# Kernel tuning notes

Hardware: AMD Instinct MI355X
Metric: run time of the kernel (lower is better)

The kernel has to match this reference:

```python
import jax, jax.numpy as jnp
import numpy as np

N_SVC, N_NODE, N_POD = 50000, 20000, 100000
F = 128          # svc/instance/node feature dims (all 128 per init_kwargs)
HID = 128        # hidden_size
OUT = 64         # out_channel
E_SVC, E_PN, E_NP = 1600000, 100000, 100000


def _graph_conv(x, src, dst, n_src, n_dst, W, b):
    """DGL GraphConv with norm='both': D_dst^{-1/2} A D_src^{-1/2} X W + b."""
    ones = jnp.ones(src.shape[0], dtype=x.dtype)
    deg_src = jnp.clip(jax.ops.segment_sum(ones, src, num_segments=n_src), 1.0)
    deg_dst = jnp.clip(jax.ops.segment_sum(ones, dst, num_segments=n_dst), 1.0)
    # normalize at source, gather, scatter-sum to dst, normalize at dst
    h = x * jax.lax.rsqrt(deg_src)[:, None]          # [n_src, F]
    msg = h[src]                                      # [E, F] gather (memory-bound)
    agg = jax.ops.segment_sum(msg, dst, num_segments=n_dst)  # [n_dst, F]
    agg = agg * jax.lax.rsqrt(deg_dst)[:, None]
    return agg @ W + b                                # [n_dst, HID]


def _leaky(h):
    return jnp.where(h > 0, h, 0.01 * h)


def setup_inputs() -> dict:
    key = jax.random.key(0)
    ks = jax.random.split(key, 16)
    d = {
        "x_svc": jax.random.normal(ks[0], (N_SVC, F), jnp.float32),
        "x_pod": jax.random.normal(ks[1], (N_POD, F), jnp.float32),
        "x_node": jax.random.normal(ks[2], (N_NODE, F), jnp.float32),
        "svc_src": jax.random.randint(ks[3], (E_SVC,), 0, N_SVC, jnp.int32),
        "svc_dst": jax.random.randint(ks[4], (E_SVC,), 0, N_SVC, jnp.int32),
        "pod_node_src": jax.random.randint(ks[5], (E_PN,), 0, N_POD, jnp.int32),
        "pod_node_dst": jax.random.randint(ks[6], (E_PN,), 0, N_NODE, jnp.int32),
        "node_pod_src": jax.random.randint(ks[7], (E_NP,), 0, N_NODE, jnp.int32),
        "node_pod_dst": jax.random.randint(ks[8], (E_NP,), 0, N_POD, jnp.int32),
        # GraphConv weights per edge type
        "W_call": jax.random.normal(ks[9], (F, HID), jnp.float32) * (1.0 / np.sqrt(F)),
        "b_call": jnp.zeros((HID,), jnp.float32),
        "W_in": jax.random.normal(ks[10], (F, HID), jnp.float32) * (1.0 / np.sqrt(F)),
        "b_in": jnp.zeros((HID,), jnp.float32),
        "W_ni": jax.random.normal(ks[11], (F, HID), jnp.float32) * (1.0 / np.sqrt(F)),
        "b_ni": jnp.zeros((HID,), jnp.float32),
        # per-node-type output Linear (hidden -> out_channel)
        "W_lin_svc": jax.random.normal(ks[12], (HID, OUT), jnp.float32) * (1.0 / np.sqrt(HID)),
        "b_lin_svc": jnp.zeros((OUT,), jnp.float32),
        "W_lin_node": jax.random.normal(ks[13], (HID, OUT), jnp.float32) * (1.0 / np.sqrt(HID)),
        "b_lin_node": jnp.zeros((OUT,), jnp.float32),
        "W_lin_pod": jax.random.normal(ks[14], (HID, OUT), jnp.float32) * (1.0 / np.sqrt(HID)),
        "b_lin_pod": jnp.zeros((OUT,), jnp.float32),
    }
    return d


def reference(x_svc, x_pod, x_node,
              svc_src, svc_dst, pod_node_src, pod_node_dst,
              node_pod_src, node_pod_dst,
              W_call, b_call, W_in, b_in, W_ni, b_ni,
              W_lin_svc, b_lin_svc, W_lin_node, b_lin_node,
              W_lin_pod, b_lin_pod):
    # HeteroGraphConv (sum aggregate; each dst type receives one edge type here)
    h_svc = _graph_conv(x_svc, svc_src, svc_dst, N_SVC, N_SVC, W_call, b_call)
    h_node = _graph_conv(x_pod, pod_node_src, pod_node_dst, N_POD, N_NODE, W_in, b_in)
    h_pod = _graph_conv(x_node, node_pod_src, node_pod_dst, N_NODE, N_POD, W_ni, b_ni)
    # per-node-type LeakyReLU + Linear
    o_svc = _leaky(h_svc) @ W_lin_svc + b_lin_svc    # [N_SVC, OUT]
    o_node = _leaky(h_node) @ W_lin_node + b_lin_node  # [N_NODE, OUT]
    o_pod = _leaky(h_pod) @ W_lin_pod + b_lin_pod    # [N_POD, OUT]
    return jnp.concatenate([o_svc, o_node, o_pod], axis=0)  # [N_SVC+N_NODE+N_POD, OUT]
```

## Files before the change

kernel.cpp:

```cpp
#include <hip/hip_runtime.h>

typedef __attribute__((ext_vector_type(8))) short short8;
typedef __attribute__((ext_vector_type(4))) float floatx4;

#define N_SVC  50000
#define N_NODE 20000
#define N_POD  100000
#define E_SVC  1600000
#define E_PN   100000
#define E_NP   100000
#define N_TOT  170000
#define E_TOT  1800000
#define NBUCK  1329
#define NBLK   128
#define PER_BLK 14063
#define P_SVC_BASE  0
#define P_NODE_BASE 50048
#define P_POD_BASE  70080
#define P_TOT       170112

__device__ __forceinline__ unsigned short f2bf(float f) {
  union { float f; unsigned u; } v; v.f = f;
  unsigned r = v.u + 0x7FFFu + ((v.u >> 16) & 1u);
  return (unsigned short)(r >> 16);
}
__device__ __forceinline__ unsigned pack_bf2(float a, float b) {
  return (unsigned)f2bf(a) | ((unsigned)f2bf(b) << 16);
}
__device__ __forceinline__ float bfl(unsigned u) { union { unsigned u; float f; } v; v.u = u << 16; return v.f; }
__device__ __forceinline__ float bfh(unsigned u) { union { unsigned u; float f; } v; v.u = u & 0xFFFF0000u; return v.f; }

__device__ __forceinline__ int dbase_of(int b) {
  if (b <= 391) return b * 6144;
  if (b <= 547) return 2402304 + (b - 391) * 1536;
  return 2641920 + (b - 547) * 512;
}
#define DST_CAP_TOT 3042304
__device__ __forceinline__ int sbase_of(int b) {
  if (b <= 391) return b * 6144;
  if (b <= 1171) return 2402304 + (b - 391) * 512;
  return 2801664 + (b - 1171) * 1536;
}
#define SRC_CAP_TOT 3044352

__device__ __forceinline__ void load_edge(int i,
    const int* __restrict__ svcS, const int* __restrict__ svcD,
    const int* __restrict__ pnS, const int* __restrict__ pnD,
    const int* __restrict__ npS, const int* __restrict__ npD,
    int& S, int& D) {
  if (i < E_SVC)             { S = svcS[i];                         D = svcD[i]; }
  else if (i < E_SVC + E_PN) { int j = i - E_SVC;        S = pnS[j] + 50000;  D = pnD[j] + 50000; }
  else                       { int j = i - E_SVC - E_PN; S = npS[j] + 150000; D = npD[j] + 70000; }
}

__global__ void init_cur(int* __restrict__ dcur, int* __restrict__ scur) {
  int b = blockIdx.x * 1024 + threadIdx.x;
  if (b < NBUCK) { dcur[b] = dbase_of(b); scur[b] = sbase_of(b); }
}

__global__ __launch_bounds__(1024) void scatter_onepass(
    const int* __restrict__ svcS, const int* __restrict__ svcD,
    const int* __restrict__ pnS, const int* __restrict__ pnD,
    const int* __restrict__ npS, const int* __restrict__ npD,
    int* __restrict__ dcur, int* __restrict__ scur,
    unsigned* __restrict__ dstbuf, unsigned char* __restrict__ srcbuf) {
  __shared__ int ldc[NBUCK], lsc[NBUCK];
  const int tid = threadIdx.x;
  for (int t = tid; t < NBUCK; t += 1024) { ldc[t] = 0; lsc[t] = 0; }
  __syncthreads();
  const int lo = blockIdx.x * PER_BLK;
  const int hi = (lo + PER_BLK < E_TOT) ? lo + PER_BLK : E_TOT;
  int Sv[14], Dv[14];
  #pragma unroll
  for (int k = 0; k < 14; ++k) {
    int e = lo + tid + k * 1024;
    if (e < hi) {
      load_edge(e, svcS, svcD, pnS, pnD, npS, npD, Sv[k], Dv[k]);
      atomicAdd(&ldc[Dv[k] >> 7], 1);
      atomicAdd(&lsc[Sv[k] >> 7], 1);
    } else Sv[k] = -1;
  }
  __syncthreads();
  for (int t = tid; t < NBUCK; t += 1024) {
    int c = ldc[t];  ldc[t] = c ? atomicAdd(&dcur[t], c) : 0;
    int c2 = lsc[t]; lsc[t] = c2 ? atomicAdd(&scur[t], c2) : 0;
  }
  __syncthreads();
  #pragma unroll
  for (int k = 0; k < 14; ++k) {
    if (Sv[k] >= 0) {
      int p = atomicAdd(&ldc[Dv[k] >> 7], 1);
      dstbuf[p] = ((unsigned)(Dv[k] & 127) << 18) | (unsigned)Sv[k];
      int q = atomicAdd(&lsc[Sv[k] >> 7], 1);
      srcbuf[q] = (unsigned char)(Sv[k] & 127);
    }
  }
}

__global__ __launch_bounds__(256) void finalize_all(
    const int* __restrict__ dcur, const int* __restrict__ scur,
    const unsigned* __restrict__ dstbuf, const unsigned char* __restrict__ srcbuf,
    int2* __restrict__ rowrange, int* __restrict__ csr, int* __restrict__ cnt_src) {
  __shared__ int lcnt[128], lcur[128];
  __shared__ int s_w0;
  const int tid = threadIdx.x;
  if (blockIdx.x < NBUCK) {
    const int b = blockIdx.x;
    const int base = dbase_of(b);
    const int cnt = dcur[b] - base;
    if (tid < 128) lcnt[tid] = 0;
    __syncthreads();
    for (int e = tid; e < cnt; e += 256) atomicAdd(&lcnt[dstbuf[base + e] >> 18], 1);
    __syncthreads();
    int excl = 0, v = 0;
    if (tid < 128) {
      v = lcnt[tid];
      int lane = tid & 63;
      int x = v;
      #pragma unroll
      for (int off = 1; off < 64; off <<= 1) {
        int y = __shfl_up(x, off, 64);
        if (lane >= off) x += y;
      }
      excl = x - v;
      if (tid == 63) s_w0 = x;
    }
    __syncthreads();
    if (tid < 128) {
      if (tid >= 64) excl += s_w0;
      lcur[tid] = excl;
      int u = b * 128 + tid;
      if (u < N_TOT) rowrange[u] = make_int2(base + excl, base + excl + v);
    }
    __syncthreads();
    for (int e = tid; e < cnt; e += 256) {
      unsigned wv = dstbuf[base + e];
      int p = atomicAdd(&lcur[wv >> 18], 1);
      csr[base + p] = (int)(wv & 0x3FFFFu);
    }
  } else {
    const int b = blockIdx.x - NBUCK;
    const int base = sbase_of(b);
    const int cnt = scur[b] - base;
    if (tid < 128) lcnt[tid] = 0;
    __syncthreads();
    for (int e = tid; e < cnt; e += 256) atomicAdd(&lcnt[srcbuf[base + e]], 1);
    __syncthreads();
    if (tid < 128) {
      int u = b * 128 + tid;
      if (u < N_TOT) cnt_src[u] = lcnt[tid];
    }
  }
}

__global__ void normalize_cast(const float* __restrict__ xs, const float* __restrict__ xp,
                               const float* __restrict__ xn, const int* __restrict__ cs,
                               unsigned* __restrict__ Xn) {
  int i = blockIdx.x * blockDim.x + threadIdx.x;
  if (i >= N_TOT * 64) return;
  int row = i >> 6, c2 = i & 63;
  const float* src;
  if (row < 50000)       src = xs + (size_t)row * 128;
  else if (row < 150000) src = xp + (size_t)(row - 50000) * 128;
  else                   src = xn + (size_t)(row - 150000) * 128;
  int cc = cs[row]; if (cc < 1) cc = 1;
  float r = rsqrtf((float)cc);
  float2 v = ((const float2*)src)[c2];
  Xn[(size_t)row * 64 + c2] = pack_bf2(v.x * r, v.y * r);
}

#define ACC8(v) { a0 += bfl(v.x); a1 += bfh(v.x); a2 += bfl(v.y); a3 += bfh(v.y); \
                  a4 += bfl(v.z); a5 += bfh(v.z); a6 += bfl(v.w); a7 += bfh(v.w); }

__global__ __launch_bounds__(256) void aggregate_bf16(
    const unsigned* __restrict__ Xn, const int2* __restrict__ rowrange,
    const int* __restrict__ csr, unsigned* __restrict__ aggb) {
  int gw = (blockIdx.x * 256 + threadIdx.x) >> 6;
  int lane = threadIdx.x & 63;
  if (gw >= P_TOT) return;
  int u; bool valid;
  if (gw < P_NODE_BASE)     { u = gw;      valid = gw < 50000; }
  else if (gw < P_POD_BASE) { u = gw - 48; valid = (gw - P_NODE_BASE) < 20000; }
  else                      { u = gw - 80; valid = (gw - P_POD_BASE) < 100000; }
  const int grp = lane >> 4, l16 = lane & 15;
  unsigned* orow = aggb + (size_t)gw * 64 + l16 * 4;
  if (!valid) {
    if (grp == 0) *(uint4*)orow = (uint4){0u, 0u, 0u, 0u};
    return;
  }
  int2 rr = rowrange[u];
  int beg = rr.x, end = rr.y;
  int deg = end - beg;
  float a0 = 0.f, a1 = 0.f, a2 = 0.f, a3 = 0.f, a4 = 0.f, a5 = 0.f, a6 = 0.f, a7 = 0.f;
  const unsigned* Xb = Xn + l16 * 4;
  int e = beg;
  for (; e + 8 <= end; e += 8) {
    int sA = csr[e + grp];
    int sB = csr[e + 4 + grp];
    uint4 vA = *(const uint4*)(Xb + (unsigned)sA * 64);
    uint4 vB = *(const uint4*)(Xb + (unsigned)sB * 64);
    ACC8(vA) ACC8(vB)
  }
  for (; e + 4 <= end; e += 4) {
    int s = csr[e + grp];
    uint4 v = *(const uint4*)(Xb + (unsigned)s * 64);
    ACC8(v)
  }
  if (grp < end - e) {
    int s = csr[e + grp];
    uint4 v = *(const uint4*)(Xb + (unsigned)s * 64);
    ACC8(v)
  }
  a0 += __shfl_xor(a0, 32, 64); a1 += __shfl_xor(a1, 32, 64);
  a2 += __shfl_xor(a2, 32, 64); a3 += __shfl_xor(a3, 32, 64);
  a4 += __shfl_xor(a4, 32, 64); a5 += __shfl_xor(a5, 32, 64);
  a6 += __shfl_xor(a6, 32, 64); a7 += __shfl_xor(a7, 32, 64);
  a0 += __shfl_xor(a0, 16, 64); a1 += __shfl_xor(a1, 16, 64);
  a2 += __shfl_xor(a2, 16, 64); a3 += __shfl_xor(a3, 16, 64);
  a4 += __shfl_xor(a4, 16, 64); a5 += __shfl_xor(a5, 16, 64);
  a6 += __shfl_xor(a6, 16, 64); a7 += __shfl_xor(a7, 16, 64);
  float rd = rsqrtf((float)(deg < 1 ? 1 : deg));
  if (grp == 0) {
    uint4 o;
    o.x = pack_bf2(a0 * rd, a1 * rd);
    o.y = pack_bf2(a2 * rd, a3 * rd);
    o.z = pack_bf2(a4 * rd, a5 * rd);
    o.w = pack_bf2(a6 * rd, a7 * rd);
    *(uint4*)orow = o;
  }
}

__global__ void wprep(const float* __restrict__ W0, const float* __restrict__ W1,
                      const float* __restrict__ W2, const float* __restrict__ L0,
                      const float* __restrict__ L1, const float* __restrict__ L2,
                      unsigned short* __restrict__ Wt, unsigned short* __restrict__ Wt2) {
  int i = blockIdx.x * 256 + threadIdx.x;
  if (i < 3 * 16384) {
    int t = i / 16384, r = i % 16384, n = r / 128, k = r % 128;
    const float* W = (t == 0) ? W0 : ((t == 1) ? W1 : W2);
    Wt[i] = f2bf(W[k * 128 + n]);
  } else if (i < 3 * 16384 + 3 * 8192) {
    int j = i - 3 * 16384;
    int t = j / 8192, r = j % 8192, n = r / 128, k = r % 128;
    const float* L = (t == 0) ? L0 : ((t == 1) ? L1 : L2);
    Wt2[j] = f2bf(L[k * 64 + n]);
  }
}

__global__ __launch_bounds__(256) void gemm_fused(
    const unsigned short* __restrict__ aggb,
    const unsigned short* __restrict__ Wt,
    const unsigned short* __restrict__ Wt2,
    const float* __restrict__ b0, const float* __restrict__ b1, const float* __restrict__ b2,
    const float* __restrict__ l0, const float* __restrict__ l1, const float* __restrict__ l2,
    float* __restrict__ out) {
  __shared__ __align__(16) unsigned short sW1[128 * 136];
  __shared__ __align__(16) unsigned short sH[4][16 * 136];
  const int bid = blockIdx.x;
  int t, bl, nb, ntile, padbase, outbase, mcnt;
  if (bid < 226)      { t = 0; bl = bid;       nb = 226; ntile = 782;  padbase = P_SVC_BASE;  outbase = 0;     mcnt = 50000; }
  else if (bid < 316) { t = 1; bl = bid - 226; nb = 90;  ntile = 313;  padbase = P_NODE_BASE; outbase = 50000; mcnt = 20000; }
  else                { t = 2; bl = bid - 316; nb = 452; ntile = 1563; padbase = P_POD_BASE;  outbase = 70000; mcnt = 100000; }
  const float* bp = (t == 0) ? b0 : ((t == 1) ? b1 : b2);
  const float* lp = (t == 0) ? l0 : ((t == 1) ? l1 : l2);

  const unsigned short* W1g = Wt + t * 16384;
  for (int uu = threadIdx.x; uu < 2048; uu += 256) {
    short8 v = *(const short8*)(W1g + uu * 8);
    *(short8*)(&sW1[(uu >> 4) * 136 + (uu & 15) * 8]) = v;
  }
  const int wv = threadIdx.x >> 6, lane = threadIdx.x & 63;
  const int quad = lane >> 4, l16 = lane & 15;

  const unsigned short* W2g = Wt2 + t * 8192;
  short8 w2f[4][4];
  #pragma unroll
  for (int n = 0; n < 4; n++)
    #pragma unroll
    for (int kt = 0; kt < 4; kt++)
      w2f[n][kt] = *(const short8*)(W2g + (n * 16 + l16) * 128 + kt * 32 + quad * 8);
  float bias1[8], bias2[4];
  #pragma unroll
  for (int n = 0; n < 8; n++) bias1[n] = bp[n * 16 + l16];
  #pragma unroll
  for (int n = 0; n < 4; n++) bias2[n] = lp[n * 16 + l16];
  __syncthreads();

  for (int tile = bl; tile < ntile; tile += nb) {
    const unsigned short* Arow = aggb + (size_t)(padbase + tile * 64 + wv * 16 + l16) * 128;
    floatx4 acc[8];
    #pragma unroll
    for (int n = 0; n < 8; n++) acc[n] = (floatx4){0.f, 0.f, 0.f, 0.f};
    #pragma unroll
    for (int kt = 0; kt < 4; kt++) {
      short8 af = *(const short8*)(Arow + kt * 32 + quad * 8);
      #pragma unroll
      for (int n = 0; n < 8; n++) {
        short8 bf = *(const short8*)(&sW1[(n * 16 + l16) * 136 + kt * 32 + quad * 8]);
        acc[n] = __builtin_amdgcn_mfma_f32_16x16x32_bf16(af, bf, acc[n], 0, 0, 0);
      }
    }
    #pragma unroll
    for (int n = 0; n < 8; n++) {
      #pragma unroll
      for (int i = 0; i < 4; i++) {
        float h = acc[n][i] + bias1[n];
        h = (h > 0.f) ? h : 0.01f * h;
        sH[wv][(quad * 4 + i) * 136 + n * 16 + l16] = f2bf(h);
      }
    }
    floatx4 acc2[4];
    #pragma unroll
    for (int n = 0; n < 4; n++) acc2[n] = (floatx4){0.f, 0.f, 0.f, 0.f};
    #pragma unroll
    for (int kt = 0; kt < 4; kt++) {
      short8 af = *(const short8*)(&sH[wv][l16 * 136 + kt * 32 + quad * 8]);
      #pragma unroll
      for (int n = 0; n < 4; n++)
        acc2[n] = __builtin_amdgcn_mfma_f32_16x16x32_bf16(af, w2f[n][kt], acc2[n], 0, 0, 0);
    }
    int r0 = tile * 64 + wv * 16 + quad * 4;
    #pragma unroll
    for (int n = 0; n < 4; n++) {
      #pragma unroll
      for (int i = 0; i < 4; i++) {
        int r = r0 + i;
        if (r < mcnt) out[(size_t)(outbase + r) * 64 + n * 16 + l16] = acc2[n][i] + bias2[n];
      }
    }
  }
}

extern "C" void kernel_launch(void* const* d_in, const int* in_sizes, int n_in,
                              void* d_out, int out_size, void* d_ws, size_t ws_size,
                              hipStream_t stream) {
  const float* x_svc  = (const float*)d_in[0];
  const float* x_pod  = (const float*)d_in[1];
  const float* x_node = (const float*)d_in[2];
  const int* svc_src  = (const int*)d_in[3];
  const int* svc_dst  = (const int*)d_in[4];
  const int* pn_src   = (const int*)d_in[5];
  const int* pn_dst   = (const int*)d_in[6];
  const int* np_src   = (const int*)d_in[7];
  const int* np_dst   = (const int*)d_in[8];
  const float* W_call = (const float*)d_in[9];
  const float* b_call = (const float*)d_in[10];
  const float* W_in   = (const float*)d_in[11];
  const float* b_in   = (const float*)d_in[12];
  const float* W_ni   = (const float*)d_in[13];
  const float* b_ni   = (const float*)d_in[14];
  const float* W_ls   = (const float*)d_in[15];
  const float* b_ls   = (const float*)d_in[16];
  const float* W_ln   = (const float*)d_in[17];
  const float* b_ln   = (const float*)d_in[18];
  const float* W_lp   = (const float*)d_in[19];
  const float* b_lp   = (const float*)d_in[20];
  float* out = (float*)d_out;

  char* ws = (char*)d_ws;
  int*  dcur     = (int*)(ws + 0);
  int*  scur     = (int*)(ws + 5504);
  int2* rowrange = (int2*)(ws + 11008);
  int*  cnt_src  = (int*)(ws + 1371008);
  int*  csr      = (int*)(ws + 2051072);
  unsigned short* Wt  = (unsigned short*)(ws + 14220288);
  unsigned short* Wt2 = (unsigned short*)(ws + 14318592);
  unsigned* Xn   = (unsigned*)(ws + 14367744);
  unsigned* dstbuf = (unsigned*)(ws + 57887744);
  unsigned char* srcbuf = (unsigned char*)(ws + 70056960);
  unsigned* aggb = (unsigned*)(ws + 73101312);

  aggb = (unsigned*)(ws + 57887744);

  aggb   = (unsigned*)(ws + 51951616);
  dstbuf = (unsigned*)(ws + 51951616);
  srcbuf = (unsigned char*)(ws + 64120832);
  Xn     = (unsigned*)(ws + 14367744);
  dstbuf = (unsigned*)(ws + 14367744);
  srcbuf = (unsigned char*)(ws + 26537088);
  aggb   = (unsigned*)(ws + 57887744);

  if (ws_size < 101436416) {
  }

  init_cur<<<2, 1024, 0, stream>>>(dcur, scur);
  scatter_onepass<<<NBLK, 1024, 0, stream>>>(svc_src, svc_dst, pn_src, pn_dst,
                                             np_src, np_dst, dcur, scur, dstbuf, srcbuf);
  finalize_all<<<2 * NBUCK, 256, 0, stream>>>(dcur, scur, dstbuf, srcbuf,
                                              rowrange, csr, cnt_src);
  wprep<<<288, 256, 0, stream>>>(W_call, W_in, W_ni, W_ls, W_ln, W_lp, Wt, Wt2);
  normalize_cast<<<42500, 256, 0, stream>>>(x_svc, x_pod, x_node, cnt_src, Xn);
  aggregate_bf16<<<(P_TOT + 3) / 4, 256, 0, stream>>>(Xn, rowrange, csr, aggb);
  gemm_fused<<<768, 256, 0, stream>>>((const unsigned short*)aggb, Wt, Wt2,
                                      b_call, b_in, b_ni, b_ls, b_ln, b_lp, out);
}
```

Baseline: 332.0 us.

## Count source degrees with global atomics, drop src bucket pass, unroll aggregation

Source-degree counting no longer goes through a bucketed byte buffer and a second finalize pass. Each edge now does a direct global atomicAdd into cnt_src, and that array is zeroed in a new init kernel. The scatter kernel also uses twice as many blocks with half the edges each, and the aggregation loop is unrolled to 16 edges using nontemporal loads and stores. The aim is to remove the srcbuf write/read traffic and the extra finalize blocks, at the cost of 1.8M contended global atomics.

```diff
diff --git a/kernel.cpp b/kernel.cpp
--- a/kernel.cpp
+++ b/kernel.cpp
@@ -2,6 +2,7 @@
 
 typedef __attribute__((ext_vector_type(8))) short short8;
 typedef __attribute__((ext_vector_type(4))) float floatx4;
+typedef __attribute__((ext_vector_type(4))) unsigned uintx4;
 
 #define N_SVC  50000
 #define N_NODE 20000
@@ -12,8 +13,8 @@
 #define N_TOT  170000
 #define E_TOT  1800000
 #define NBUCK  1329
-#define NBLK   128
-#define PER_BLK 14063
+#define NBLK   256
+#define PER_BLK 7032
 #define P_SVC_BASE  0
 #define P_NODE_BASE 50048
 #define P_POD_BASE  70080
@@ -36,12 +37,6 @@
   return 2641920 + (b - 547) * 512;
 }
 #define DST_CAP_TOT 3042304
-__device__ __forceinline__ int sbase_of(int b) {
-  if (b <= 391) return b * 6144;
-  if (b <= 1171) return 2402304 + (b - 391) * 512;
-  return 2801664 + (b - 1171) * 1536;
-}
-#define SRC_CAP_TOT 3044352
 
 __device__ __forceinline__ void load_edge(int i,
     const int* __restrict__ svcS, const int* __restrict__ svcD,
@@ -53,103 +48,87 @@
   else                       { int j = i - E_SVC - E_PN; S = npS[j] + 150000; D = npD[j] + 70000; }
 }
 
-__global__ void init_cur(int* __restrict__ dcur, int* __restrict__ scur) {
-  int b = blockIdx.x * 1024 + threadIdx.x;
-  if (b < NBUCK) { dcur[b] = dbase_of(b); scur[b] = sbase_of(b); }
+__global__ __launch_bounds__(1024) void init_buffers(int* __restrict__ dcur,
+                                                     int* __restrict__ cnt_src) {
+  int i = blockIdx.x * 1024 + threadIdx.x;
+  if (i < NBUCK) dcur[i] = dbase_of(i);
+  if (i < N_TOT) cnt_src[i] = 0;
 }
 
 __global__ __launch_bounds__(1024) void scatter_onepass(
     const int* __restrict__ svcS, const int* __restrict__ svcD,
     const int* __restrict__ pnS, const int* __restrict__ pnD,
     const int* __restrict__ npS, const int* __restrict__ npD,
-    int* __restrict__ dcur, int* __restrict__ scur,
-    unsigned* __restrict__ dstbuf, unsigned char* __restrict__ srcbuf) {
-  __shared__ int ldc[NBUCK], lsc[NBUCK];
+    int* __restrict__ dcur, int* __restrict__ cnt_src,
+    unsigned* __restrict__ dstbuf) {
+  __shared__ int ldc[NBUCK];
   const int tid = threadIdx.x;
-  for (int t = tid; t < NBUCK; t += 1024) { ldc[t] = 0; lsc[t] = 0; }
+  for (int t = tid; t < NBUCK; t += 1024) ldc[t] = 0;
   __syncthreads();
   const int lo = blockIdx.x * PER_BLK;
   const int hi = (lo + PER_BLK < E_TOT) ? lo + PER_BLK : E_TOT;
-  int Sv[14], Dv[14];
-  #pragma unroll
-  for (int k = 0; k < 14; ++k) {
+  int Sv[7], Dv[7];
+  #pragma unroll
+  for (int k = 0; k < 7; ++k) {
     int e = lo + tid + k * 1024;
     if (e < hi) {
       load_edge(e, svcS, svcD, pnS, pnD, npS, npD, Sv[k], Dv[k]);
       atomicAdd(&ldc[Dv[k] >> 7], 1);
-      atomicAdd(&lsc[Sv[k] >> 7], 1);
+      atomicAdd(&cnt_src[Sv[k]], 1);
     } else Sv[k] = -1;
   }
   __syncthreads();
   for (int t = tid; t < NBUCK; t += 1024) {
-    int c = ldc[t];  ldc[t] = c ? atomicAdd(&dcur[t], c) : 0;
-    int c2 = lsc[t]; lsc[t] = c2 ? atomicAdd(&scur[t], c2) : 0;
-  }
-  __syncthreads();
-  #pragma unroll
-  for (int k = 0; k < 14; ++k) {
+    int c = ldc[t]; ldc[t] = c ? atomicAdd(&dcur[t], c) : 0;
+  }
+  __syncthreads();
+  #pragma unroll
+  for (int k = 0; k < 7; ++k) {
     if (Sv[k] >= 0) {
       int p = atomicAdd(&ldc[Dv[k] >> 7], 1);
       dstbuf[p] = ((unsigned)(Dv[k] & 127) << 18) | (unsigned)Sv[k];
-      int q = atomicAdd(&lsc[Sv[k] >> 7], 1);
-      srcbuf[q] = (unsigned char)(Sv[k] & 127);
-    }
-  }
-}
-
-__global__ __launch_bounds__(256) void finalize_all(
-    const int* __restrict__ dcur, const int* __restrict__ scur,
-    const unsigned* __restrict__ dstbuf, const unsigned char* __restrict__ srcbuf,
-    int2* __restrict__ rowrange, int* __restrict__ csr, int* __restrict__ cnt_src) {
+    }
+  }
+}
+
+__global__ __launch_bounds__(256) void finalize_dst(
+    const int* __restrict__ dcur, const unsigned* __restrict__ dstbuf,
+    int2* __restrict__ rowrange, int* __restrict__ csr) {
   __shared__ int lcnt[128], lcur[128];
   __shared__ int s_w0;
   const int tid = threadIdx.x;
-  if (blockIdx.x < NBUCK) {
-    const int b = blockIdx.x;
-    const int base = dbase_of(b);
-    const int cnt = dcur[b] - base;
-    if (tid < 128) lcnt[tid] = 0;
-    __syncthreads();
-    for (int e = tid; e < cnt; e += 256) atomicAdd(&lcnt[dstbuf[base + e] >> 18], 1);
-    __syncthreads();
-    int excl = 0, v = 0;
-    if (tid < 128) {
-      v = lcnt[tid];
-      int lane = tid & 63;
-      int x = v;
-      #pragma unroll
-      for (int off = 1; off < 64; off <<= 1) {
-        int y = __shfl_up(x, off, 64);
-        if (lane >= off) x += y;
-      }
-      excl = x - v;
-      if (tid == 63) s_w0 = x;
-    }
-    __syncthreads();
-    if (tid < 128) {
-      if (tid >= 64) excl += s_w0;
-      lcur[tid] = excl;
-      int u = b * 128 + tid;
-      if (u < N_TOT) rowrange[u] = make_int2(base + excl, base + excl + v);
-    }
-    __syncthreads();
-    for (int e = tid; e < cnt; e += 256) {
-      unsigned wv = dstbuf[base + e];
-      int p = atomicAdd(&lcur[wv >> 18], 1);
-      csr[base + p] = (int)(wv & 0x3FFFFu);
-    }
-  } else {
-    const int b = blockIdx.x - NBUCK;
-    const int base = sbase_of(b);
-    const int cnt = scur[b] - base;
-    if (tid < 128) lcnt[tid] = 0;
-    __syncthreads();
-    for (int e = tid; e < cnt; e += 256) atomicAdd(&lcnt[srcbuf[base + e]], 1);
-    __syncthreads();
-    if (tid < 128) {
-      int u = b * 128 + tid;
-      if (u < N_TOT) cnt_src[u] = lcnt[tid];
-    }
+  const int b = blockIdx.x;
+  const int base = dbase_of(b);
+  const int cnt = dcur[b] - base;
+  if (tid < 128) lcnt[tid] = 0;
+  __syncthreads();
+  for (int e = tid; e < cnt; e += 256) atomicAdd(&lcnt[dstbuf[base + e] >> 18], 1);
+  __syncthreads();
+  int excl = 0, v = 0;
+  if (tid < 128) {
+    v = lcnt[tid];
+    int lane = tid & 63;
+    int x = v;
+    #pragma unroll
+    for (int off = 1; off < 64; off <<= 1) {
+      int y = __shfl_up(x, off, 64);
+      if (lane >= off) x += y;
+    }
+    excl = x - v;
+    if (tid == 63) s_w0 = x;
+  }
+  __syncthreads();
+  if (tid < 128) {
+    if (tid >= 64) excl += s_w0;
+    lcur[tid] = excl;
+    int u = b * 128 + tid;
+    if (u < N_TOT) rowrange[u] = make_int2(base + excl, base + excl + v);
+  }
+  __syncthreads();
+  for (int e = tid; e < cnt; e += 256) {
+    unsigned wv = dstbuf[base + e];
+    int p = atomicAdd(&lcur[wv >> 18], 1);
+    csr[base + p] = (int)(wv & 0x3FFFFu);
   }
 }
 
@@ -185,7 +164,7 @@
   const int grp = lane >> 4, l16 = lane & 15;
   unsigned* orow = aggb + (size_t)gw * 64 + l16 * 4;
   if (!valid) {
-    if (grp == 0) *(uint4*)orow = (uint4){0u, 0u, 0u, 0u};
+    if (grp == 0) __builtin_nontemporal_store((uintx4){0u, 0u, 0u, 0u}, (uintx4*)orow);
     return;
   }
   int2 rr = rowrange[u];
@@ -194,20 +173,31 @@
   float a0 = 0.f, a1 = 0.f, a2 = 0.f, a3 = 0.f, a4 = 0.f, a5 = 0.f, a6 = 0.f, a7 = 0.f;
   const unsigned* Xb = Xn + l16 * 4;
   int e = beg;
+  for (; e + 16 <= end; e += 16) {
+    int sA = __builtin_nontemporal_load(csr + e + grp);
+    int sB = __builtin_nontemporal_load(csr + e + 4 + grp);
+    int sC = __builtin_nontemporal_load(csr + e + 8 + grp);
+    int sD = __builtin_nontemporal_load(csr + e + 12 + grp);
+    uint4 vA = *(const uint4*)(Xb + (unsigned)sA * 64);
+    uint4 vB = *(const uint4*)(Xb + (unsigned)sB * 64);
+    uint4 vC = *(const uint4*)(Xb + (unsigned)sC * 64);
+    uint4 vD = *(const uint4*)(Xb + (unsigned)sD * 64);
+    ACC8(vA) ACC8(vB) ACC8(vC) ACC8(vD)
+  }
   for (; e + 8 <= end; e += 8) {
-    int sA = csr[e + grp];
-    int sB = csr[e + 4 + grp];
+    int sA = __builtin_nontemporal_load(csr + e + grp);
+    int sB = __builtin_nontemporal_load(csr + e + 4 + grp);
     uint4 vA = *(const uint4*)(Xb + (unsigned)sA * 64);
     uint4 vB = *(const uint4*)(Xb + (unsigned)sB * 64);
     ACC8(vA) ACC8(vB)
   }
   for (; e + 4 <= end; e += 4) {
-    int s = csr[e + grp];
+    int s = __builtin_nontemporal_load(csr + e + grp);
     uint4 v = *(const uint4*)(Xb + (unsigned)s * 64);
     ACC8(v)
   }
   if (grp < end - e) {
-    int s = csr[e + grp];
+    int s = __builtin_nontemporal_load(csr + e + grp);
     uint4 v = *(const uint4*)(Xb + (unsigned)s * 64);
     ACC8(v)
   }
@@ -221,12 +211,12 @@
   a6 += __shfl_xor(a6, 16, 64); a7 += __shfl_xor(a7, 16, 64);
   float rd = rsqrtf((float)(deg < 1 ? 1 : deg));
   if (grp == 0) {
-    uint4 o;
+    uintx4 o;
     o.x = pack_bf2(a0 * rd, a1 * rd);
     o.y = pack_bf2(a2 * rd, a3 * rd);
     o.z = pack_bf2(a4 * rd, a5 * rd);
     o.w = pack_bf2(a6 * rd, a7 * rd);
-    *(uint4*)orow = o;
+    __builtin_nontemporal_store(o, (uintx4*)orow);
   }
 }
 
@@ -359,35 +349,19 @@
 
   char* ws = (char*)d_ws;
   int*  dcur     = (int*)(ws + 0);
-  int*  scur     = (int*)(ws + 5504);
   int2* rowrange = (int2*)(ws + 11008);
   int*  cnt_src  = (int*)(ws + 1371008);
   int*  csr      = (int*)(ws + 2051072);
   unsigned short* Wt  = (unsigned short*)(ws + 14220288);
   unsigned short* Wt2 = (unsigned short*)(ws + 14318592);
-  unsigned* Xn   = (unsigned*)(ws + 14367744);
-  unsigned* dstbuf = (unsigned*)(ws + 57887744);
-  unsigned char* srcbuf = (unsigned char*)(ws + 70056960);
-  unsigned* aggb = (unsigned*)(ws + 73101312);
-
-  aggb = (unsigned*)(ws + 57887744);
-
-  aggb   = (unsigned*)(ws + 51951616);
-  dstbuf = (unsigned*)(ws + 51951616);
-  srcbuf = (unsigned char*)(ws + 64120832);
-  Xn     = (unsigned*)(ws + 14367744);
-  dstbuf = (unsigned*)(ws + 14367744);
-  srcbuf = (unsigned char*)(ws + 26537088);
-  aggb   = (unsigned*)(ws + 57887744);
-
-  if (ws_size < 101436416) {
-  }
-
-  init_cur<<<2, 1024, 0, stream>>>(dcur, scur);
+  unsigned* Xn     = (unsigned*)(ws + 14367744);
+  unsigned* dstbuf = (unsigned*)(ws + 14367744);
+  unsigned* aggb   = (unsigned*)(ws + 57887744);
+
+  init_buffers<<<167, 1024, 0, stream>>>(dcur, cnt_src);
   scatter_onepass<<<NBLK, 1024, 0, stream>>>(svc_src, svc_dst, pn_src, pn_dst,
-                                             np_src, np_dst, dcur, scur, dstbuf, srcbuf);
-  finalize_all<<<2 * NBUCK, 256, 0, stream>>>(dcur, scur, dstbuf, srcbuf,
-                                              rowrange, csr, cnt_src);
+                                             np_src, np_dst, dcur, cnt_src, dstbuf);
+  finalize_dst<<<NBUCK, 256, 0, stream>>>(dcur, dstbuf, rowrange, csr);
   wprep<<<288, 256, 0, stream>>>(W_call, W_in, W_ni, W_ls, W_ln, W_lp, Wt, Wt2);
   normalize_cast<<<42500, 256, 0, stream>>>(x_svc, x_pod, x_node, cnt_src, Xn);
   aggregate_bf16<<<(P_TOT + 3) / 4, 256, 0, stream>>>(Xn, rowrange, csr, aggb);
```

Result: slower. 398.1 us (+19.9%).
